# Performance work log

Measured on AMD Instinct MI355X. Metric: run time of the kernel, lower is better.

The kernel has to match this reference:

```python
import jax, jax.numpy as jnp
import numpy as np

DIM = 128      # input node feature dim
GS = 64        # SAGEConv output dim
AF = 32        # additional (ir_score) feature dim
NB = 2         # nb_classes
G = 8192       # num_graphs in batch
NPG = 16       # nodes per graph
N = G * NPG    # total nodes = 131072
E = 2097152    # total edges (avg degree 16)


def setup_inputs() -> dict:
    key = jax.random.key(0)
    ks = jax.random.split(key, 10)

    def w(k, shape, fan_in):
        return jax.random.normal(k, shape, jnp.float32) / np.sqrt(fan_in)

    return {
        "x": jax.random.normal(ks[0], (N, DIM), jnp.float32),
        "edge_index": jax.random.randint(ks[1], (2, E), 0, N),
        "set_indices": jax.random.randint(ks[2], (G, 2), 0, NPG),
        "batch_ids": jnp.repeat(jnp.arange(G), NPG),  # sorted graph ids, PyG style
        "ir_score": jax.random.uniform(ks[3], (G, AF), jnp.float32),
        "W_l": w(ks[4], (DIM, GS), DIM),
        "b_l": jnp.zeros((GS,), jnp.float32),
        "W_r": w(ks[5], (DIM, GS), DIM),
        "W_ir": w(ks[6], (AF, 2 * GS), AF),
        "b_ir": jnp.zeros((2 * GS,), jnp.float32),
        "W1": w(ks[7], ((2 * GS) * (2 * GS), 200), (2 * GS) * (2 * GS)),
        "b1": jnp.zeros((200,), jnp.float32),
        "W2": w(ks[8], (200, NB), 200),
        "b2": jnp.zeros((NB,), jnp.float32),
    }


def reference(x, edge_index, set_indices, batch_ids, ir_score,
              W_l, b_l, W_r, W_ir, b_ir, W1, b1, W2, b2):
    n = x.shape[0]
    src, dst = edge_index[0], edge_index[1]

    # SAGEConv (mean aggregation): out = lin_l(mean_{j in N(i)} x_j) + lin_r(x_i)
    agg = jax.ops.segment_sum(x[src], dst, num_segments=n)           # [N, DIM]
    deg = jax.ops.segment_sum(jnp.ones((src.shape[0],), x.dtype), dst, num_segments=n)
    mean = agg / jnp.maximum(deg, 1.0)[:, None]
    h = jax.nn.relu(mean @ W_l + b_l + x @ W_r)                      # [N, GS]

    # per-graph node counts -> index bases (cumsum), then global pair indices
    g = set_indices.shape[0]
    num_nodes = jax.ops.segment_sum(jnp.ones((n,), jnp.float32), batch_ids, num_segments=g)
    csum = jnp.cumsum(num_nodes.astype(jnp.int64))
    index_bases = jnp.concatenate([jnp.zeros((1,), jnp.int64), csum[:-1]])
    sib = index_bases[:, None] + set_indices                         # [G, 2]

    pair = h[sib].reshape(g, 2 * GS)                                 # gather + flatten

    # fusion: relu(linear(ir_score)) then per-graph outer product
    S = jax.nn.relu(ir_score @ W_ir + b_ir)                          # [G, 2*GS]
    outer = jnp.einsum('gi,gj->gij', pair, S).reshape(g, -1)         # [G, (2GS)^2]

    # decode MLP
    z = jax.nn.relu(outer @ W1 + b1)                                 # [G, 200]
    logits = z @ W2 + b2                                             # [G, NB]
    return logits
```

## Files before the change

kernel.cpp:

```cpp
#include <hip/hip_runtime.h>

#define NN   131072
#define GG   8192
#define EE   2097152
#define KBIG 16384
#define NPAD 208
#define NSPLIT 8
#define NSEL  16384
#define SBUCK 256
#define SUBC  4
#define SCAPS 336
#define SCAPT (SUBC*SCAPS)

typedef _Float16 half_t;
typedef __attribute__((ext_vector_type(8))) _Float16 half8;
typedef __attribute__((ext_vector_type(4))) float floatx4;

__device__ inline floatx4 mfma16(half8 a, half8 b, floatx4 c) {
  return __builtin_amdgcn_mfma_f32_16x16x32_f16(a, b, c, 0, 0, 0);
}

__global__ void prep_w(const float* __restrict__ Wl, const float* __restrict__ Wr,
                       half_t* __restrict__ Wt) {
  int idx = blockIdx.x * blockDim.x + threadIdx.x;
  int n = idx >> 7, k = idx & 127;
  float v = (n < 64) ? Wl[k * 64 + n] : Wr[k * 64 + (n - 64)];
  Wt[n * 128 + k] = (half_t)v;
}
__global__ void prep_w1p(const float* __restrict__ W1, half_t* __restrict__ W1p) {
  int idx = blockIdx.x * blockDim.x + threadIdx.x;
  int lane = idx & 63;
  int t = idx >> 6;
  int nt = t % 13; t /= 13;
  int jc = t & 3;  t >>= 2;
  int i  = t & 15; t >>= 4;
  int split = t;
  int n = nt * 16 + (lane & 15);
  int k0 = split * 2048 + i * 128 + jc * 32 + (lane >> 4) * 8;
  half8 v;
#pragma unroll
  for (int e = 0; e < 8; e++)
    v[e] = (half_t)((n < 200) ? W1[(size_t)(k0 + e) * 200 + n] : 0.f);
  *(half8*)(W1p + (size_t)idx * 8) = v;
}

__global__ void set_slots(const int* __restrict__ set_idx, int* __restrict__ nodemap,
                          int* __restrict__ slot_node) {
  int idx = blockIdx.x * blockDim.x + threadIdx.x;
  int g = idx >> 1, which = idx & 1;
  int node = g * 16 + set_idx[g * 2 + which];
  slot_node[idx] = node;
  nodemap[node] = idx;
}

__global__ void filter_scatter(const int* __restrict__ src, const int* __restrict__ dst,
                               const int* __restrict__ nodemap,
                               int* __restrict__ scnt, unsigned int* __restrict__ sbuf) {
  int e = blockIdx.x * blockDim.x + threadIdx.x;
  int d = dst[e];
  int slot = nodemap[d];
  if (slot >= 0) {
    int b = slot >> 6;
    int sub = blockIdx.x & (SUBC - 1);
    int pos = atomicAdd(&scnt[(b * SUBC + sub) * 16], 1);
    if (pos < SCAPS)
      sbuf[(size_t)(b * SUBC + sub) * SCAPS + pos] =
          (unsigned int)src[e] | ((unsigned int)(slot & 63) << 17);
  }
}

__global__ __launch_bounds__(256) void yr_gemm(const float* __restrict__ x,
                                               const half_t* __restrict__ Wt,
                                               const float* __restrict__ b_l,
                                               half_t* __restrict__ y16,
                                               half_t* __restrict__ r16) {
  int tid = threadIdx.x, w = tid >> 6, lane = tid & 63;
  int m = lane & 15, kc = (lane >> 4) * 8;
  int node0 = blockIdx.x * 64 + w * 16;
  floatx4 acc[8];
#pragma unroll
  for (int nt = 0; nt < 8; nt++) acc[nt] = (floatx4){0.f, 0.f, 0.f, 0.f};
#pragma unroll
  for (int step = 0; step < 4; step++) {
    int k0 = step * 32 + kc;
    const float* xp = x + (size_t)(node0 + m) * 128 + k0;
    float4 u0 = *(const float4*)xp;
    float4 u1 = *(const float4*)(xp + 4);
    half8 av = {(half_t)u0.x, (half_t)u0.y, (half_t)u0.z, (half_t)u0.w,
                (half_t)u1.x, (half_t)u1.y, (half_t)u1.z, (half_t)u1.w};
#pragma unroll
    for (int nt = 0; nt < 8; nt++) {
      half8 bv = *(const half8*)(Wt + (nt * 16 + m) * 128 + k0);
      acc[nt] = mfma16(av, bv, acc[nt]);
    }
  }
  int col = lane & 15, rb = (lane >> 4) * 4;
#pragma unroll
  for (int nt = 0; nt < 8; nt++) {
    int n = nt * 16 + col;
    float bias = (n >= 64) ? b_l[n - 64] : 0.f;
#pragma unroll
    for (int r = 0; r < 4; r++) {
      int row = node0 + rb + r;
      float v = acc[nt][r] + bias;
      if (n < 64) y16[(size_t)row * 64 + n] = (half_t)v;
      else        r16[(size_t)row * 64 + (n - 64)] = (half_t)v;
    }
  }
}

__global__ __launch_bounds__(256) void slot_agg(const unsigned int* __restrict__ sbuf,
                                                const int* __restrict__ scnt,
                                                const int* __restrict__ slot_node,
                                                const half_t* __restrict__ y16,
                                                const half_t* __restrict__ r16,
                                                half_t* __restrict__ h_slot) {
  __shared__ int sorted[SCAPT];
  __shared__ int hist[64];
  __shared__ int base[64];
  __shared__ int start[65];
  int b = blockIdx.x, tid = threadIdx.x;
  if (tid < 64) hist[tid] = 0;
  __syncthreads();
  unsigned int myedge[2 * SUBC];
  int mycnt = 0;
#pragma unroll
  for (int sub = 0; sub < SUBC; sub++) {
    int n = scnt[(b * SUBC + sub) * 16]; if (n > SCAPS) n = SCAPS;
    const unsigned int* eb = sbuf + (size_t)(b * SUBC + sub) * SCAPS;
    for (int e = tid; e < n; e += 256) {
      unsigned int pk = eb[e];
      myedge[mycnt++] = pk;
      atomicAdd(&hist[pk >> 17], 1);
    }
  }
  __syncthreads();
  if (tid < 64) {
    int v = hist[tid];
    int sum = v;
#pragma unroll
    for (int off = 1; off < 64; off <<= 1) {
      int u = __shfl_up(sum, off);
      if (tid >= off) sum += u;
    }
    start[tid] = sum - v;
    base[tid]  = sum - v;
    if (tid == 63) start[64] = sum;
  }
  __syncthreads();
  for (int i = 0; i < mycnt; i++) {
    unsigned int pk = myedge[i];
    int pos = atomicAdd(&base[pk >> 17], 1);
    sorted[pos] = (int)(pk & 0x1FFFF);
  }
  __syncthreads();
  int s = tid >> 2, p = tid & 3;
  int e0 = start[s], e1 = start[s + 1];
  float acc[16];
#pragma unroll
  for (int j = 0; j < 16; j++) acc[j] = 0.f;
  int e = e0;
  for (; e + 2 <= e1; e += 2) {
    int s0 = sorted[e], s1 = sorted[e + 1];
    const half8* p0 = (const half8*)(y16 + (size_t)s0 * 64 + p * 16);
    const half8* p1 = (const half8*)(y16 + (size_t)s1 * 64 + p * 16);
    half8 a0 = p0[0], c0 = p0[1], a1 = p1[0], c1 = p1[1];
#pragma unroll
    for (int j = 0; j < 8; j++) {
      acc[j]     += (float)a0[j] + (float)a1[j];
      acc[8 + j] += (float)c0[j] + (float)c1[j];
    }
  }
  if (e < e1) {
    int s0 = sorted[e];
    const half8* p0 = (const half8*)(y16 + (size_t)s0 * 64 + p * 16);
    half8 a0 = p0[0], c0 = p0[1];
#pragma unroll
    for (int j = 0; j < 8; j++) { acc[j] += (float)a0[j]; acc[8 + j] += (float)c0[j]; }
  }
  int slot = b * 64 + s;
  int node = slot_node[slot];
  float inv = 1.0f / fmaxf((float)(e1 - e0), 1.0f);
  const half8* rr = (const half8*)(r16 + (size_t)node * 64 + p * 16);
  half8 r0 = rr[0], r1 = rr[1];
  half8 o0, o1;
#pragma unroll
  for (int j = 0; j < 8; j++) {
    o0[j] = (half_t)fmaxf(acc[j] * inv + (float)r0[j], 0.f);
    o1[j] = (half_t)fmaxf(acc[8 + j] * inv + (float)r1[j], 0.f);
  }
  half8* hp = (half8*)(h_slot + (size_t)slot * 64 + p * 16);
  hp[0] = o0;
  hp[1] = o1;
}

__global__ void s_pair_kernel(const float* __restrict__ ir, const float* __restrict__ W_ir,
                              const float* __restrict__ b_ir, half_t* __restrict__ S16,
                              const half_t* __restrict__ h_slot,
                              const int* __restrict__ nodemap,
                              const int* __restrict__ set_idx, half_t* __restrict__ pair16) {
  int idx = blockIdx.x * blockDim.x + threadIdx.x;
  int g = idx >> 7, o = idx & 127;
  const float* irow = ir + g * 32;
  float sv = b_ir[o];
#pragma unroll
  for (int a = 0; a < 32; a++) sv += irow[a] * W_ir[a * 128 + o];
  S16[idx] = (half_t)fmaxf(sv, 0.f);
  int which = o >> 6, c = o & 63;
  int node = g * 16 + set_idx[g * 2 + which];
  int slot = nodemap[node];
  pair16[idx] = h_slot[(size_t)slot * 64 + c];
}

__global__ __launch_bounds__(256, 2) void biggemm(const half_t* __restrict__ pair16,
                                                  const half_t* __restrict__ S16,
                                                  const half_t* __restrict__ W1p,
                                                  float* __restrict__ zpart) {
  __shared__ half_t bbuf[2][26 * 512];
  __shared__ half_t pls[16][128];
  int bx = blockIdx.x;
  int mt = bx >> 3, split = bx & 7;
  int g0 = mt * 128;
  int tid = threadIdx.x, w = tid >> 6, lane = tid & 63;
  int m = lane & 15, q = lane >> 4, kc = q * 8;

  auto stage = [&](int ii, int halfsel, int bufsel) {
#pragma unroll
    for (int ff = 0; ff < 7; ff++) {
      int f = ff * 4 + w;
      if (f < 26) {
        const half_t* gsrc = W1p + (((size_t)(split * 16 + ii) * 52) + halfsel * 26 + f) * 512 + lane * 8;
        half_t* ldst = &bbuf[bufsel][f * 512];
        __builtin_amdgcn_global_load_lds((const __attribute__((address_space(1))) uint32_t*)gsrc,
                                         (__attribute__((address_space(3))) uint32_t*)ldst, 16, 0, 0);
      }
    }
  };

  stage(0, 0, 0);

  {
    int row = tid & 127, sel = tid >> 7;
    half8 pa = *(const half8*)(pair16 + (size_t)(g0 + row) * 128 + split * 16 + sel * 8);
#pragma unroll
    for (int j = 0; j < 8; j++) pls[sel * 8 + j][row] = pa[j];
  }

  half8 sf[2][4];
#pragma unroll
  for (int sub = 0; sub < 2; sub++) {
    int grow = g0 + w * 32 + sub * 16 + m;
#pragma unroll
    for (int jc = 0; jc < 4; jc++)
      sf[sub][jc] = *(const half8*)(S16 + (size_t)grow * 128 + jc * 32 + kc);
  }

  floatx4 acc[2][13];
#pragma unroll
  for (int sb = 0; sb < 2; sb++)
#pragma unroll
    for (int nt = 0; nt < 13; nt++) acc[sb][nt] = (floatx4){0.f, 0.f, 0.f, 0.f};

  for (int i = 0; i < 16; i++) {
    half_t p0, p1;
#pragma unroll
    for (int h2 = 0; h2 < 2; h2++) {
      __syncthreads();
      if (h2 == 0) {
        p0 = pls[i][w * 32 + 0 * 16 + m];
        p1 = pls[i][w * 32 + 1 * 16 + m];
        stage(i, 1, 1);
      } else if (i < 15) {
        stage(i + 1, 0, 0);
      }
      const half_t* bb = bbuf[h2];
#pragma unroll
      for (int jj = 0; jj < 2; jj++) {
        const int jc = h2 * 2 + jj;
        half8 a0 = sf[0][jc] * p0;
        half8 a1 = sf[1][jc] * p1;
#pragma unroll
        for (int nt = 0; nt < 13; nt++) {
          half8 bv = *(const half8*)(bb + (jj * 13 + nt) * 512 + lane * 8);
          acc[0][nt] = mfma16(a0, bv, acc[0][nt]);
          acc[1][nt] = mfma16(a1, bv, acc[1][nt]);
        }
      }
    }
  }

#pragma unroll
  for (int sub = 0; sub < 2; sub++)
#pragma unroll
    for (int nt = 0; nt < 13; nt++)
#pragma unroll
      for (int r = 0; r < 4; r++) {
        int row = g0 + w * 32 + sub * 16 + q * 4 + r;
        zpart[((size_t)split * GG + row) * NPAD + nt * 16 + m] = acc[sub][nt][r];
      }
}

__global__ __launch_bounds__(256) void reduce_mlp(const float* __restrict__ zpart,
                                                  const float* __restrict__ b1,
                                                  const float* __restrict__ W2,
                                                  const float* __restrict__ b2,
                                                  float* __restrict__ out) {
  int tid = threadIdx.x;
  int w = tid >> 6, lane = tid & 63;
  int g = blockIdx.x * 4 + w;
  float p0 = 0.f, p1 = 0.f;
#pragma unroll
  for (int qq = 0; qq < 4; qq++) {
    int c = qq * 64 + lane;
    if (c < 200) {
      float z = 0.f;
#pragma unroll
      for (int sp = 0; sp < NSPLIT; sp++)
        z += zpart[((size_t)sp * GG + g) * NPAD + c];
      z += b1[c];
      z = fmaxf(z, 0.f);
      p0 += z * W2[c * 2];
      p1 += z * W2[c * 2 + 1];
    }
  }
#pragma unroll
  for (int off = 32; off; off >>= 1) {
    p0 += __shfl_down(p0, off);
    p1 += __shfl_down(p1, off);
  }
  if (lane == 0) {
    out[g * 2] = p0 + b2[0];
    out[g * 2 + 1] = p1 + b2[1];
  }
}

extern "C" void kernel_launch(void* const* d_in, const int* in_sizes, int n_in,
                              void* d_out, int out_size, void* d_ws, size_t ws_size,
                              hipStream_t stream) {
  const float* x     = (const float*)d_in[0];
  const int*   ei    = (const int*)d_in[1];
  const int*   setix = (const int*)d_in[2];
  const float* ir    = (const float*)d_in[4];
  const float* W_l   = (const float*)d_in[5];
  const float* b_l   = (const float*)d_in[6];
  const float* W_r   = (const float*)d_in[7];
  const float* W_ir  = (const float*)d_in[8];
  const float* b_ir  = (const float*)d_in[9];
  const float* W1    = (const float*)d_in[10];
  const float* b1    = (const float*)d_in[11];
  const float* W2    = (const float*)d_in[12];
  const float* b2    = (const float*)d_in[13];
  float* out = (float*)d_out;

  char* ws = (char*)d_ws;
  size_t off = 0;
  auto alloc = [&](size_t bytes) -> void* {
    void* p = ws + off;
    off = (off + bytes + 255) & ~(size_t)255;
    return p;
  };
  size_t pool_start = off;
  int* nodemap   = (int*)alloc((size_t)NN * 4);
  int* slot_node = (int*)alloc((size_t)NSEL * 4);
  int* scnt      = (int*)alloc((size_t)SBUCK * SUBC * 16 * 4);
  unsigned int* sbuf = (unsigned int*)alloc((size_t)SBUCK * SUBC * SCAPS * 4);
  half_t* y16    = (half_t*)alloc((size_t)NN * 64 * 2);
  half_t* r16    = (half_t*)alloc((size_t)NN * 64 * 2);
  half_t* h_slot = (half_t*)alloc((size_t)NSEL * 64 * 2);
  float* zpart = (float*)(ws + pool_start);
  {
    size_t zend = pool_start + (((size_t)NSPLIT * GG * NPAD * 4 + 255) & ~(size_t)255);
    if (off < zend) off = zend;
  }
  half_t* Wt     = (half_t*)alloc(128 * 128 * 2);
  half_t* W1p    = (half_t*)alloc((size_t)NPAD * KBIG * 2);
  half_t* S16    = (half_t*)alloc((size_t)GG * 128 * 2);
  half_t* pair16 = (half_t*)alloc((size_t)GG * 128 * 2);
  (void)ws_size; (void)in_sizes; (void)n_in; (void)out_size;

  const int* esrc = ei;
  const int* edst = ei + EE;

  hipMemsetAsync(nodemap, 0xFF, (size_t)NN * 4, stream);
  hipMemsetAsync(scnt, 0, (size_t)SBUCK * SUBC * 16 * 4, stream);

  prep_w<<<(128 * 128) / 256, 256, 0, stream>>>(W_l, W_r, Wt);
  prep_w1p<<<(NPAD * KBIG / 8) / 256, 256, 0, stream>>>(W1, W1p);

  set_slots<<<NSEL / 256, 256, 0, stream>>>(setix, nodemap, slot_node);
  filter_scatter<<<EE / 256, 256, 0, stream>>>(esrc, edst, nodemap, scnt, sbuf);

  yr_gemm<<<NN / 64, 256, 0, stream>>>(x, Wt, b_l, y16, r16);
  slot_agg<<<SBUCK, 256, 0, stream>>>(sbuf, scnt, slot_node, y16, r16, h_slot);

  s_pair_kernel<<<(GG * 128) / 256, 256, 0, stream>>>(ir, W_ir, b_ir, S16, h_slot, nodemap, setix, pair16);

  biggemm<<<(GG / 128) * NSPLIT, 256, 0, stream>>>(pair16, S16, W1p, zpart);
  reduce_mlp<<<GG / 4, 256, 0, stream>>>(zpart, b1, W2, b2, out);
}
```

Measured before the change: 287.7 us.

## Retile big GEMM to 2x2 wave grid with N padded to 224

Changes the biggemm wave decomposition from each wave owning 32 rows across all 13 N-tiles to a 2x2 grid where each wave owns 64 rows and 7 of 14 N-tiles. Each B fragment read from LDS now feeds four MFMAs instead of two, which raises LDS reuse and cuts LDS read traffic per MFMA. In exchange, N is padded from 208 to 224, adding about 8% of wasted MFMA work and W1p/zpart storage. The S register fragments also grow to four sub-tiles per wave, which increases register pressure.

```diff
diff --git a/kernel.cpp b/kernel.cpp
--- a/kernel.cpp
+++ b/kernel.cpp
@@ -4,7 +4,7 @@
 #define GG   8192
 #define EE   2097152
 #define KBIG 16384
-#define NPAD 208
+#define NPAD 224
 #define NSPLIT 8
 #define NSEL  16384
 #define SBUCK 256
@@ -31,7 +31,7 @@
   int idx = blockIdx.x * blockDim.x + threadIdx.x;
   int lane = idx & 63;
   int t = idx >> 6;
-  int nt = t % 13; t /= 13;
+  int nt = t % 14; t /= 14;
   int jc = t & 3;  t >>= 2;
   int i  = t & 15; t >>= 4;
   int split = t;
@@ -216,24 +216,24 @@
                                                   const half_t* __restrict__ S16,
                                                   const half_t* __restrict__ W1p,
                                                   float* __restrict__ zpart) {
-  __shared__ half_t bbuf[2][26 * 512];
+  __shared__ half_t bbuf[2][28 * 512];
   __shared__ half_t pls[16][128];
   int bx = blockIdx.x;
   int mt = bx >> 3, split = bx & 7;
   int g0 = mt * 128;
   int tid = threadIdx.x, w = tid >> 6, lane = tid & 63;
+  int wm = w >> 1, wn = w & 1;
   int m = lane & 15, q = lane >> 4, kc = q * 8;
+  int ntb = wn * 7;
 
   auto stage = [&](int ii, int halfsel, int bufsel) {
 #pragma unroll
     for (int ff = 0; ff < 7; ff++) {
       int f = ff * 4 + w;
-      if (f < 26) {
-        const half_t* gsrc = W1p + (((size_t)(split * 16 + ii) * 52) + halfsel * 26 + f) * 512 + lane * 8;
-        half_t* ldst = &bbuf[bufsel][f * 512];
-        __builtin_amdgcn_global_load_lds((const __attribute__((address_space(1))) uint32_t*)gsrc,
-                                         (__attribute__((address_space(3))) uint32_t*)ldst, 16, 0, 0);
-      }
+      const half_t* gsrc = W1p + (((size_t)(split * 16 + ii) * 56) + halfsel * 28 + f) * 512 + lane * 8;
+      half_t* ldst = &bbuf[bufsel][f * 512];
+      __builtin_amdgcn_global_load_lds((const __attribute__((address_space(1))) uint32_t*)gsrc,
+                                       (__attribute__((address_space(3))) uint32_t*)ldst, 16, 0, 0);
     }
   };
 
@@ -246,29 +246,31 @@
     for (int j = 0; j < 8; j++) pls[sel * 8 + j][row] = pa[j];
   }
 
-  half8 sf[2][4];
-#pragma unroll
-  for (int sub = 0; sub < 2; sub++) {
-    int grow = g0 + w * 32 + sub * 16 + m;
+  half8 sf[4][4];
+#pragma unroll
+  for (int sub = 0; sub < 4; sub++) {
+    int grow = g0 + wm * 64 + sub * 16 + m;
 #pragma unroll
     for (int jc = 0; jc < 4; jc++)
       sf[sub][jc] = *(const half8*)(S16 + (size_t)grow * 128 + jc * 32 + kc);
   }
 
-  floatx4 acc[2][13];
-#pragma unroll
-  for (int sb = 0; sb < 2; sb++)
-#pragma unroll
-    for (int nt = 0; nt < 13; nt++) acc[sb][nt] = (floatx4){0.f, 0.f, 0.f, 0.f};
+  floatx4 acc[4][7];
+#pragma unroll
+  for (int sb = 0; sb < 4; sb++)
+#pragma unroll
+    for (int t = 0; t < 7; t++) acc[sb][t] = (floatx4){0.f, 0.f, 0.f, 0.f};
 
   for (int i = 0; i < 16; i++) {
-    half_t p0, p1;
+    half_t p0, p1, p2, p3;
 #pragma unroll
     for (int h2 = 0; h2 < 2; h2++) {
       __syncthreads();
       if (h2 == 0) {
-        p0 = pls[i][w * 32 + 0 * 16 + m];
-        p1 = pls[i][w * 32 + 1 * 16 + m];
+        p0 = pls[i][wm * 64 + 0 * 16 + m];
+        p1 = pls[i][wm * 64 + 1 * 16 + m];
+        p2 = pls[i][wm * 64 + 2 * 16 + m];
+        p3 = pls[i][wm * 64 + 3 * 16 + m];
         stage(i, 1, 1);
       } else if (i < 15) {
         stage(i + 1, 0, 0);
@@ -279,24 +281,28 @@
         const int jc = h2 * 2 + jj;
         half8 a0 = sf[0][jc] * p0;
         half8 a1 = sf[1][jc] * p1;
-#pragma unroll
-        for (int nt = 0; nt < 13; nt++) {
-          half8 bv = *(const half8*)(bb + (jj * 13 + nt) * 512 + lane * 8);
-          acc[0][nt] = mfma16(a0, bv, acc[0][nt]);
-          acc[1][nt] = mfma16(a1, bv, acc[1][nt]);
+        half8 a2 = sf[2][jc] * p2;
+        half8 a3 = sf[3][jc] * p3;
+#pragma unroll
+        for (int t = 0; t < 7; t++) {
+          half8 bv = *(const half8*)(bb + (jj * 14 + ntb + t) * 512 + lane * 8);
+          acc[0][t] = mfma16(a0, bv, acc[0][t]);
+          acc[1][t] = mfma16(a1, bv, acc[1][t]);
+          acc[2][t] = mfma16(a2, bv, acc[2][t]);
+          acc[3][t] = mfma16(a3, bv, acc[3][t]);
         }
       }
     }
   }
 
 #pragma unroll
-  for (int sub = 0; sub < 2; sub++)
-#pragma unroll
-    for (int nt = 0; nt < 13; nt++)
+  for (int sub = 0; sub < 4; sub++)
+#pragma unroll
+    for (int t = 0; t < 7; t++)
 #pragma unroll
       for (int r = 0; r < 4; r++) {
-        int row = g0 + w * 32 + sub * 16 + q * 4 + r;
-        zpart[((size_t)split * GG + row) * NPAD + nt * 16 + m] = acc[sub][nt][r];
+        int row = g0 + wm * 64 + sub * 16 + q * 4 + r;
+        zpart[((size_t)split * GG + row) * NPAD + (ntb + t) * 16 + m] = acc[sub][t][r];
       }
 }
 
```

Result: slower. 332.7 us (+15.7%).

## Compute root projection only for selected slots and stage weights in LDS

Applied to the files above, without the earlier changes.

Splits the combined projection GEMM in two. A y-only GEMM over all nodes covers the neighbor projection, and a small r_slots kernel computes the root projection only for the selected slot nodes, so the full-size r16 array is no longer computed or written. The y GEMM stages its weight half into LDS through global_load_lds and writes coalesced half8 rows through a shared buffer. This adds one kernel launch and a gathered read of x rows for the slots.

```diff
diff --git a/kernel.cpp b/kernel.cpp
--- a/kernel.cpp
+++ b/kernel.cpp
@@ -69,51 +69,101 @@
   }
 }
 
-__global__ __launch_bounds__(256) void yr_gemm(const float* __restrict__ x,
-                                               const half_t* __restrict__ Wt,
+__global__ __launch_bounds__(256) void y_gemm(const float* __restrict__ x,
+                                              const half_t* __restrict__ WtG,
+                                              half_t* __restrict__ y16) {
+  __shared__ half_t wlds[64 * 128];
+  __shared__ half_t ybuf[64 * 72];
+  int tid = threadIdx.x, w = tid >> 6, lane = tid & 63;
+  int m = lane & 15, q = lane >> 4, kc = q * 8;
+#pragma unroll
+  for (int it = 0; it < 4; it++) {
+    int cb = (it * 4 + w) * 64;
+    const half_t* g = WtG + ((size_t)cb + lane) * 8;
+    half_t* l = wlds + (size_t)cb * 8;
+    __builtin_amdgcn_global_load_lds((const __attribute__((address_space(1))) uint32_t*)g,
+                                     (__attribute__((address_space(3))) uint32_t*)l, 16, 0, 0);
+  }
+  int node0 = blockIdx.x * 64 + w * 16;
+  float4 xu[4][2];
+#pragma unroll
+  for (int step = 0; step < 4; step++) {
+    const float* xp = x + (size_t)(node0 + m) * 128 + step * 32 + kc;
+    xu[step][0] = *(const float4*)xp;
+    xu[step][1] = *(const float4*)(xp + 4);
+  }
+  __syncthreads();
+  floatx4 acc[4];
+#pragma unroll
+  for (int nt = 0; nt < 4; nt++) acc[nt] = (floatx4){0.f, 0.f, 0.f, 0.f};
+#pragma unroll
+  for (int step = 0; step < 4; step++) {
+    float4 u0 = xu[step][0], u1 = xu[step][1];
+    half8 av = {(half_t)u0.x, (half_t)u0.y, (half_t)u0.z, (half_t)u0.w,
+                (half_t)u1.x, (half_t)u1.y, (half_t)u1.z, (half_t)u1.w};
+    int k0 = step * 32 + kc;
+#pragma unroll
+    for (int nt = 0; nt < 4; nt++) {
+      half8 bv = *(const half8*)(wlds + (nt * 16 + m) * 128 + k0);
+      acc[nt] = mfma16(av, bv, acc[nt]);
+    }
+  }
+#pragma unroll
+  for (int nt = 0; nt < 4; nt++)
+#pragma unroll
+    for (int r = 0; r < 4; r++)
+      ybuf[(w * 16 + q * 4 + r) * 72 + nt * 16 + m] = (half_t)acc[nt][r];
+  __syncthreads();
+#pragma unroll
+  for (int c = tid; c < 512; c += 256) {
+    int row = c >> 3, co = (c & 7) * 8;
+    *(half8*)(y16 + (size_t)(blockIdx.x * 64 + row) * 64 + co) =
+        *(const half8*)(ybuf + row * 72 + co);
+  }
+}
+
+__global__ __launch_bounds__(256) void r_slots(const float* __restrict__ x,
+                                               const half_t* __restrict__ WtG,
                                                const float* __restrict__ b_l,
-                                               half_t* __restrict__ y16,
-                                               half_t* __restrict__ r16) {
+                                               const int* __restrict__ slot_node,
+                                               half_t* __restrict__ r_slot) {
   int tid = threadIdx.x, w = tid >> 6, lane = tid & 63;
-  int m = lane & 15, kc = (lane >> 4) * 8;
-  int node0 = blockIdx.x * 64 + w * 16;
-  floatx4 acc[8];
-#pragma unroll
-  for (int nt = 0; nt < 8; nt++) acc[nt] = (floatx4){0.f, 0.f, 0.f, 0.f};
+  int m = lane & 15, q = lane >> 4, kc = q * 8;
+  int s0 = blockIdx.x * 64 + w * 16;
+  int node = slot_node[s0 + m];
+  floatx4 acc[4];
+#pragma unroll
+  for (int nt = 0; nt < 4; nt++) acc[nt] = (floatx4){0.f, 0.f, 0.f, 0.f};
 #pragma unroll
   for (int step = 0; step < 4; step++) {
     int k0 = step * 32 + kc;
-    const float* xp = x + (size_t)(node0 + m) * 128 + k0;
+    const float* xp = x + (size_t)node * 128 + k0;
     float4 u0 = *(const float4*)xp;
     float4 u1 = *(const float4*)(xp + 4);
     half8 av = {(half_t)u0.x, (half_t)u0.y, (half_t)u0.z, (half_t)u0.w,
                 (half_t)u1.x, (half_t)u1.y, (half_t)u1.z, (half_t)u1.w};
 #pragma unroll
-    for (int nt = 0; nt < 8; nt++) {
-      half8 bv = *(const half8*)(Wt + (nt * 16 + m) * 128 + k0);
+    for (int nt = 0; nt < 4; nt++) {
+      half8 bv = *(const half8*)(WtG + (size_t)(64 + nt * 16 + m) * 128 + k0);
       acc[nt] = mfma16(av, bv, acc[nt]);
     }
   }
-  int col = lane & 15, rb = (lane >> 4) * 4;
-#pragma unroll
-  for (int nt = 0; nt < 8; nt++) {
-    int n = nt * 16 + col;
-    float bias = (n >= 64) ? b_l[n - 64] : 0.f;
+#pragma unroll
+  for (int nt = 0; nt < 4; nt++) {
+    int n = nt * 16 + m;
+    float bias = b_l[n];
 #pragma unroll
     for (int r = 0; r < 4; r++) {
-      int row = node0 + rb + r;
-      float v = acc[nt][r] + bias;
-      if (n < 64) y16[(size_t)row * 64 + n] = (half_t)v;
-      else        r16[(size_t)row * 64 + (n - 64)] = (half_t)v;
+      int s = s0 + q * 4 + r;
+      r_slot[(size_t)s * 64 + n] = (half_t)(acc[nt][r] + bias);
     }
   }
 }
 
 __global__ __launch_bounds__(256) void slot_agg(const unsigned int* __restrict__ sbuf,
                                                 const int* __restrict__ scnt,
-                                                const int* __restrict__ slot_node,
                                                 const half_t* __restrict__ y16,
-                                                const half_t* __restrict__ r16,
+                                                const half_t* __restrict__ r_slot,
                                                 half_t* __restrict__ h_slot) {
   __shared__ int sorted[SCAPT];
   __shared__ int hist[64];
@@ -179,9 +229,8 @@
     for (int j = 0; j < 8; j++) { acc[j] += (float)a0[j]; acc[8 + j] += (float)c0[j]; }
   }
   int slot = b * 64 + s;
-  int node = slot_node[slot];
   float inv = 1.0f / fmaxf((float)(e1 - e0), 1.0f);
-  const half8* rr = (const half8*)(r16 + (size_t)node * 64 + p * 16);
+  const half8* rr = (const half8*)(r_slot + (size_t)slot * 64 + p * 16);
   half8 r0 = rr[0], r1 = rr[1];
   half8 o0, o1;
 #pragma unroll
@@ -365,7 +414,7 @@
   int* scnt      = (int*)alloc((size_t)SBUCK * SUBC * 16 * 4);
   unsigned int* sbuf = (unsigned int*)alloc((size_t)SBUCK * SUBC * SCAPS * 4);
   half_t* y16    = (half_t*)alloc((size_t)NN * 64 * 2);
-  half_t* r16    = (half_t*)alloc((size_t)NN * 64 * 2);
+  half_t* r_slot = (half_t*)alloc((size_t)NSEL * 64 * 2);
   half_t* h_slot = (half_t*)alloc((size_t)NSEL * 64 * 2);
   float* zpart = (float*)(ws + pool_start);
   {
@@ -390,8 +439,9 @@
   set_slots<<<NSEL / 256, 256, 0, stream>>>(setix, nodemap, slot_node);
   filter_scatter<<<EE / 256, 256, 0, stream>>>(esrc, edst, nodemap, scnt, sbuf);
 
-  yr_gemm<<<NN / 64, 256, 0, stream>>>(x, Wt, b_l, y16, r16);
-  slot_agg<<<SBUCK, 256, 0, stream>>>(sbuf, scnt, slot_node, y16, r16, h_slot);
+  y_gemm<<<NN / 64, 256, 0, stream>>>(x, Wt, y16);
+  r_slots<<<NSEL / 64, 256, 0, stream>>>(x, Wt, b_l, slot_node, r_slot);
+  slot_agg<<<SBUCK, 256, 0, stream>>>(sbuf, scnt, y16, r_slot, h_slot);
 
   s_pair_kernel<<<(GG * 128) / 256, 256, 0, stream>>>(ir, W_ir, b_ir, S16, h_slot, nodemap, setix, pair16);
 
```

Result: faster. 257.4 us (-10.5%).
